# Performance work log

Hardware: AMD Instinct MI355X
Metric: run time of the kernel (lower is better)

## Reference

```python
import jax, jax.numpy as jnp
import numpy as np

DIM = 256
HEADS = 8
HD = DIM // HEADS  # 32
RPE_H = 512
STRIDE = 16
B, NQ = 4, 300
HH, WW = 64, 64
N = HH * WW


def setup_inputs() -> dict:
    key = jax.random.key(0)
    ks = jax.random.split(key, 24)

    def lin(k, fan_in, fan_out):
        return (jax.random.normal(k, (fan_in, fan_out), jnp.float32)
                / np.float32(np.sqrt(fan_in)))

    # boxes in absolute pixel coords (image is WW*STRIDE = 1024 px wide)
    rp_xy = jax.random.uniform(ks[0], (B, NQ, 1, 2), jnp.float32) * (WW * STRIDE)
    rp_wh = jax.random.uniform(ks[1], (B, NQ, 1, 2), jnp.float32) * 256.0 + 16.0
    reference_points = jnp.concatenate([rp_xy, rp_wh], axis=-1)  # [B,NQ,1,4]

    inp = {
        "query": jax.random.normal(ks[2], (B, NQ, DIM), jnp.float32),
        "reference_points": reference_points,
        "k_input_flatten": jax.random.normal(ks[3], (B, N, DIM), jnp.float32),
        "v_input_flatten": jax.random.normal(ks[4], (B, N, DIM), jnp.float32),
        "input_spatial_shapes": jnp.array([[HH, WW]], dtype=jnp.int32),
        "input_padding_mask": (jax.random.uniform(ks[5], (B, N)) < 0.1).astype(jnp.int32),
        # projections (stored as [in, out]; y = x @ W + b)
        "Wq": lin(ks[6], DIM, DIM), "bq": jnp.zeros((DIM,), jnp.float32),
        "Wk": lin(ks[7], DIM, DIM), "bk": jnp.zeros((DIM,), jnp.float32),
        "Wv": lin(ks[8], DIM, DIM), "bv": jnp.zeros((DIM,), jnp.float32),
        "Wp": lin(ks[9], DIM, DIM), "bp": jnp.zeros((DIM,), jnp.float32),
        # CPB MLP 1 (x-deltas): Linear(2,512)+ReLU+Linear(512,HEADS,no bias)
        "W1x": lin(ks[10], 2, RPE_H), "b1x": jnp.zeros((RPE_H,), jnp.float32),
        "W2x": lin(ks[11], RPE_H, HEADS),
        # CPB MLP 2 (y-deltas)
        "W1y": lin(ks[12], 2, RPE_H), "b1y": jnp.zeros((RPE_H,), jnp.float32),
        "W2y": lin(ks[13], RPE_H, HEADS),
    }
    return inp


def reference(query, reference_points, k_input_flatten, v_input_flatten,
              input_spatial_shapes, input_padding_mask,
              Wq, bq, Wk, bk, Wv, bv, Wp, bp,
              W1x, b1x, W2x, W1y, b1y, W2y):
    h = int(input_spatial_shapes[0, 0])
    w = int(input_spatial_shapes[0, 1])
    scale = HD ** -0.5

    # cxcywh -> (x1,y1,x2,y2)
    c, s = reference_points[..., :2], reference_points[..., 2:]
    ref_pts = jnp.concatenate([c - s / 2, c + s / 2], axis=-1)  # [B,NQ,1,4]

    pos_x = (jnp.arange(w, dtype=jnp.float32) + 0.5) * STRIDE  # [w]
    pos_y = (jnp.arange(h, dtype=jnp.float32) + 0.5) * STRIDE  # [h]
    delta_x = ref_pts[..., 0::2] - pos_x[None, None, :, None]  # [B,NQ,w,2]
    delta_y = ref_pts[..., 1::2] - pos_y[None, None, :, None]  # [B,NQ,h,2]

    rpe_x = jax.nn.relu(delta_x @ W1x + b1x) @ W2x  # [B,NQ,w,HEADS]
    rpe_y = jax.nn.relu(delta_y @ W1y + b1y) @ W2y  # [B,NQ,h,HEADS]
    rpe = rpe_x[:, :, None, :, :] + rpe_y[:, :, :, None, :]  # [B,NQ,h,w,H]

    Bq, Nq, C = query.shape
    rpe = rpe.reshape(Bq, Nq, h * w, HEADS).transpose(0, 3, 1, 2)  # [B,H,NQ,N]

    q = (query @ Wq + bq).reshape(Bq, Nq, HEADS, HD).transpose(0, 2, 1, 3) * scale
    k = (k_input_flatten @ Wk + bk).reshape(Bq, -1, HEADS, HD).transpose(0, 2, 1, 3)
    v = (v_input_flatten @ Wv + bv).reshape(Bq, -1, HEADS, HD).transpose(0, 2, 1, 3)

    attn = jnp.einsum('bhqd,bhkd->bhqk', q, k) + rpe
    attn = attn + input_padding_mask[:, None, None, :].astype(attn.dtype) * (-100.0)
    fi = jnp.finfo(attn.dtype)
    attn = jnp.clip(attn, fi.min, fi.max)
    attn = jax.nn.softmax(attn, axis=-1)

    x = jnp.einsum('bhqk,bhkd->bhqd', attn, v)
    x = x.transpose(0, 2, 1, 3).reshape(Bq, Nq, C)
    return x @ Wp + bp
```

## Files before the change

### kernel.cpp

```cpp
#include <hip/hip_runtime.h>
#include <math.h>

#define B_   4
#define NQ_  300
#define DIM_ 256
#define H_   8
#define HD_  32
#define N_   4096

typedef _Float16 f16;
typedef f16   f16x8 __attribute__((ext_vector_type(8)));
typedef f16   f16x4 __attribute__((ext_vector_type(4)));
typedef float f32x4 __attribute__((ext_vector_type(4)));

__global__ __launch_bounds__(256) void prep_wt(
    const float* __restrict__ Wq, const float* __restrict__ Wk,
    const float* __restrict__ Wv, const float* __restrict__ Wp,
    f16* __restrict__ WT, float qscale)
{
  __shared__ float t[64][65];
  const int z = blockIdx.z;
  const float* W = z == 0 ? Wq : z == 1 ? Wk : z == 2 ? Wv : Wp;
  const float s = z == 0 ? qscale : 1.0f;
  f16* O = WT + (size_t)z * 65536;
  const int k0 = blockIdx.y * 64, n0 = blockIdx.x * 64;
  const int r = threadIdx.x >> 2, c0 = (threadIdx.x & 3) * 16;
#pragma unroll
  for (int c = 0; c < 16; c += 4) {
    float4 v = *(const float4*)(W + (size_t)(k0 + r) * 256 + n0 + c0 + c);
    t[r][c0 + c] = v.x; t[r][c0 + c + 1] = v.y;
    t[r][c0 + c + 2] = v.z; t[r][c0 + c + 3] = v.w;
  }
  __syncthreads();
  f16* orow = O + (size_t)(n0 + r) * 256 + k0 + c0;
#pragma unroll
  for (int c = 0; c < 16; c += 4) {
    f16x4 p;
    p[0] = (f16)(t[c0 + c + 0][r] * s);
    p[1] = (f16)(t[c0 + c + 1][r] * s);
    p[2] = (f16)(t[c0 + c + 2][r] * s);
    p[3] = (f16)(t[c0 + c + 3][r] * s);
    *(f16x4*)(orow + c) = p;
  }
}

__device__ __forceinline__ void gemm_body(
    const void* __restrict__ Ain, const f16* __restrict__ WT,
    const float* __restrict__ bias, void* __restrict__ C,
    int M, float scale, int a_f16, int mode, int bm, int bn, int tid)
{
  __shared__ f16 As[64][40];
  __shared__ f16 Bs[64][40];
  const int lane = tid & 63;
  const int wv = tid >> 6;
  const int l15 = lane & 15, g = lane >> 4;
  const int arow = tid >> 2, akq = (tid & 3) * 8;

  f32x4 acc[4];
#pragma unroll
  for (int nt = 0; nt < 4; ++nt) acc[nt] = (f32x4){0.f, 0.f, 0.f, 0.f};

  for (int k0 = 0; k0 < 256; k0 += 32) {
    {
      const int gm = bm + arow;
      f16x8 av;
      if (gm < M) {
        if (a_f16) {
          av = *(const f16x8*)((const f16*)Ain + (size_t)gm * 256 + k0 + akq);
        } else {
          const float* ap = (const float*)Ain + (size_t)gm * 256 + k0 + akq;
          float4 a0 = *(const float4*)ap;
          float4 a1 = *(const float4*)(ap + 4);
          av[0] = (f16)a0.x; av[1] = (f16)a0.y; av[2] = (f16)a0.z; av[3] = (f16)a0.w;
          av[4] = (f16)a1.x; av[5] = (f16)a1.y; av[6] = (f16)a1.z; av[7] = (f16)a1.w;
        }
      } else {
#pragma unroll
        for (int i = 0; i < 8; ++i) av[i] = (f16)0.f;
      }
      *(f16x8*)&As[arow][akq] = av;
      *(f16x8*)&Bs[arow][akq] =
          *(const f16x8*)(WT + (size_t)(bn + arow) * 256 + k0 + akq);
    }
    __syncthreads();
    const f16x8 af = *(const f16x8*)&As[wv * 16 + l15][g * 8];
#pragma unroll
    for (int nt = 0; nt < 4; ++nt) {
      const f16x8 bf = *(const f16x8*)&Bs[nt * 16 + l15][g * 8];
      acc[nt] = __builtin_amdgcn_mfma_f32_16x16x32_f16(af, bf, acc[nt], 0, 0, 0);
    }
    __syncthreads();
  }

#pragma unroll
  for (int nt = 0; nt < 4; ++nt) {
    const int n = bn + nt * 16 + l15;
    const float bv = bias[n] * scale;
    if (mode == 2) {
      const int m0 = bm + wv * 16 + g * 4;
      const int bb = m0 >> 12, nk = m0 & 4095;
      f16x4 pk;
#pragma unroll
      for (int r = 0; r < 4; ++r) pk[r] = (f16)(acc[nt][r] + bv);
      *(f16x4*)((f16*)C + (size_t)bb * (256 * 4096) + (size_t)n * 4096 + nk) = pk;
    } else {
#pragma unroll
      for (int r = 0; r < 4; ++r) {
        const int m = bm + wv * 16 + g * 4 + r;
        if (m >= M) continue;
        const float v = acc[nt][r] + bv;
        if (mode == 0) ((float*)C)[(size_t)m * 256 + n] = v;
        else           ((f16*)C)[(size_t)m * 256 + n] = (f16)v;
      }
    }
  }
}

__global__ __launch_bounds__(256) void proj_qkv(
    const float* __restrict__ query, const float* __restrict__ kin,
    const float* __restrict__ vin, const f16* __restrict__ WT,
    const float* __restrict__ bq, const float* __restrict__ bk,
    const float* __restrict__ bv, f16* __restrict__ Qf,
    f16* __restrict__ Kf, f16* __restrict__ Vtf, float qscale)
{
  const int z = blockIdx.z;
  const int bm = blockIdx.y * 64, bn = blockIdx.x * 64;
  if (z == 0) {
    if (bm >= B_ * NQ_) return;
    gemm_body(query, WT, bq, Qf, B_ * NQ_, qscale, 0, 1, bm, bn, threadIdx.x);
  } else if (z == 1) {
    gemm_body(kin, WT + 65536, bk, Kf, B_ * N_, 1.0f, 0, 1, bm, bn, threadIdx.x);
  } else {
    gemm_body(vin, WT + 2 * 65536, bv, Vtf, B_ * N_, 1.0f, 0, 2, bm, bn, threadIdx.x);
  }
}

__global__ __launch_bounds__(256) void gemm_out(
    const f16* __restrict__ X, const f16* __restrict__ WT,
    const float* __restrict__ bp, float* __restrict__ out)
{
  gemm_body(X, WT + 3 * 65536, bp, out, B_ * NQ_, 1.0f, 1, 0,
            blockIdx.y * 64, blockIdx.x * 64, threadIdx.x);
}

__global__ __launch_bounds__(256) void rpe_kernel(
    const float* __restrict__ refpts,
    const float* __restrict__ W1x, const float* __restrict__ b1x, const float* __restrict__ W2x,
    const float* __restrict__ W1y, const float* __restrict__ b1y, const float* __restrict__ W2y,
    float* __restrict__ rpx, float* __restrict__ rpy)
{
  __shared__ float sRed[4][64][8];
  const int tid = threadIdx.x;
  const int lane = tid & 63;
  const int wv = __builtin_amdgcn_readfirstlane(tid >> 6);
  const int bq = blockIdx.x;
  const int axis = blockIdx.y;
  const float* W1 = axis ? W1y : W1x;
  const float* b1 = axis ? b1y : b1x;
  const float* W2 = axis ? W2y : W2x;
  float* out = axis ? rpy : rpx;

  const float c  = refpts[bq * 4 + axis];
  const float sz = refpts[bq * 4 + 2 + axis];
  const float pos = (lane + 0.5f) * 16.0f;
  const float d0 = c - 0.5f * sz - pos;
  const float d1 = c + 0.5f * sz - pos;
  float acc[8] = {};
  const int r0 = wv * 128;
#pragma unroll 4
  for (int i = 0; i < 128; ++i) {
    const int r = r0 + i;
    const float w10 = W1[r], w11 = W1[512 + r], bb = b1[r];
    const float hv = fmaxf(fmaf(d0, w10, fmaf(d1, w11, bb)), 0.0f);
    const float* w2r = W2 + r * 8;
#pragma unroll
    for (int hh = 0; hh < 8; ++hh) acc[hh] += hv * w2r[hh];
  }
#pragma unroll
  for (int hh = 0; hh < 8; ++hh) sRed[wv][lane][hh] = acc[hh];
  __syncthreads();
  for (int idx = tid; idx < 512; idx += 256) {
    const int jj = idx >> 3, hh = idx & 7;
    out[(size_t)bq * 512 + idx] =
        sRed[0][jj][hh] + sRed[1][jj][hh] + sRed[2][jj][hh] + sRed[3][jj][hh];
  }
}

__global__ __launch_bounds__(512) void attn_mfma(
    const f16* __restrict__ Qf, const f16* __restrict__ Kf,
    const f16* __restrict__ Vtf, const float* __restrict__ rpx,
    const float* __restrict__ rpy, const int* __restrict__ mask,
    f16* __restrict__ X)
{
  __shared__ float smask[N_];
  __shared__ float srx[16][68];
  __shared__ float sry[16][68];
  __shared__ float mO[7][8][64];
  __shared__ float mlm[7][16];
  __shared__ float mll[7][16];

  const int tid = threadIdx.x;
  const int lane = tid & 63;
  const int kh = tid >> 6;
  const int qb = blockIdx.x % 20;
  const int h  = (blockIdx.x / 20) % H_;
  const int b  = blockIdx.x / (20 * H_);
  const int q0 = qb * 16;
  const float L2E = 1.44269504f;

  {
    const int4* mm4 = (const int4*)(mask + b * N_);
    for (int i = tid; i < N_ / 4; i += 512) {
      int4 mm = mm4[i];
      smask[4 * i + 0] = -100.f * L2E * (float)mm.x;
      smask[4 * i + 1] = -100.f * L2E * (float)mm.y;
      smask[4 * i + 2] = -100.f * L2E * (float)mm.z;
      smask[4 * i + 3] = -100.f * L2E * (float)mm.w;
    }
  }
  for (int i = tid; i < 1024; i += 512) {
    int qq = i >> 6, j = i & 63;
    int qg = q0 + qq; if (qg > NQ_ - 1) qg = NQ_ - 1;
    size_t base = (size_t)(b * NQ_ + qg) * 512 + (size_t)j * 8 + h;
    srx[qq][j] = rpx[base] * L2E;
    sry[qq][j] = rpy[base] * L2E;
  }
  __syncthreads();

  const int l15 = lane & 15, g = lane >> 4;
  const int qrow = q0 + l15;
  const int qq = qrow > NQ_ - 1 ? NQ_ - 1 : qrow;

  const f16x8 qf = *(const f16x8*)(Qf + (size_t)(b * NQ_ + qq) * 256 + h * 32 + g * 8);

  f32x4 O0 = {0.f, 0.f, 0.f, 0.f}, O1 = {0.f, 0.f, 0.f, 0.f};
  float lacc = 0.f;
  float mrun = -1e30f;
  const f16* kb  = Kf + (size_t)b * N_ * 256 + h * 32 + g * 8;
  const f16* v0p = Vtf + (size_t)(b * 256 + h * 32 + l15) * N_ + g * 4;
  const f16* v1p = v0p + (size_t)16 * N_;

  for (int sp = 0; sp < 4; ++sp) {
    const int kbase = kh * 512 + sp * 128;
    f32x4 s2c[8];
    float lmax = -1e30f;
#pragma unroll
    for (int cc = 0; cc < 8; ++cc) {
      const int k0 = kbase + cc * 16;
      f16x8 kf = *(const f16x8*)(kb + (size_t)(k0 + l15) * 256);
      f32x4 S = __builtin_amdgcn_mfma_f32_16x16x32_f16(
          kf, qf, (f32x4){0.f, 0.f, 0.f, 0.f}, 0, 0, 0);
      const float ry2 = sry[l15][k0 >> 6];
      const float4 rx = *(const float4*)&srx[l15][(k0 & 63) + g * 4];
      const float4 sm = *(const float4*)&smask[k0 + g * 4];
      f32x4 s2;
      s2[0] = fmaf(S[0], L2E, rx.x + sm.x + ry2);
      s2[1] = fmaf(S[1], L2E, rx.y + sm.y + ry2);
      s2[2] = fmaf(S[2], L2E, rx.z + sm.z + ry2);
      s2[3] = fmaf(S[3], L2E, rx.w + sm.w + ry2);
      lmax = fmaxf(lmax, fmaxf(fmaxf(s2[0], s2[1]), fmaxf(s2[2], s2[3])));
      s2c[cc] = s2;
    }
    lmax = fmaxf(lmax, __shfl_xor(lmax, 16));
    lmax = fmaxf(lmax, __shfl_xor(lmax, 32));
    const float mnew = fmaxf(mrun, lmax);
    const float f = exp2f(mrun - mnew);
    mrun = mnew;
    lacc *= f;
#pragma unroll
    for (int r = 0; r < 4; ++r) { O0[r] *= f; O1[r] *= f; }
#pragma unroll
    for (int cc = 0; cc < 8; ++cc) {
      const int k0 = kbase + cc * 16;
      f16x4 pf;
      float ls = 0.f;
#pragma unroll
      for (int r = 0; r < 4; ++r) {
        const float pv = exp2f(s2c[cc][r] - mrun);
        ls += pv;
        pf[r] = (f16)pv;
      }
      lacc += ls;
      const f16x4 vf0 = *(const f16x4*)(v0p + k0);
      const f16x4 vf1 = *(const f16x4*)(v1p + k0);
      O0 = __builtin_amdgcn_mfma_f32_16x16x16f16(vf0, pf, O0, 0, 0, 0);
      O1 = __builtin_amdgcn_mfma_f32_16x16x16f16(vf1, pf, O1, 0, 0, 0);
    }
  }

  lacc += __shfl_xor(lacc, 16);
  lacc += __shfl_xor(lacc, 32);

  if (kh > 0) {
#pragma unroll
    for (int r = 0; r < 4; ++r) {
      mO[kh - 1][r][lane] = O0[r];
      mO[kh - 1][4 + r][lane] = O1[r];
    }
    if (lane < 16) {
      mlm[kh - 1][lane] = mrun;
      mll[kh - 1][lane] = lacc;
    }
  }
  __syncthreads();
  if (kh == 0) {
    float ms = mrun;
#pragma unroll
    for (int w = 0; w < 7; ++w) ms = fmaxf(ms, mlm[w][l15]);
    const float f0 = exp2f(mrun - ms);
    float lt = lacc * f0;
    float fw[7];
#pragma unroll
    for (int w = 0; w < 7; ++w) {
      fw[w] = exp2f(mlm[w][l15] - ms);
      lt += mll[w][l15] * fw[w];
    }
    const float rl = 1.0f / lt;
    if (qrow < NQ_) {
      f16* xr = X + (size_t)(b * NQ_ + qrow) * 256 + h * 32;
      f16x4 p0, p1;
#pragma unroll
      for (int r = 0; r < 4; ++r) {
        float o0 = O0[r] * f0, o1 = O1[r] * f0;
#pragma unroll
        for (int w = 0; w < 7; ++w) {
          o0 += mO[w][r][lane] * fw[w];
          o1 += mO[w][4 + r][lane] * fw[w];
        }
        p0[r] = (f16)(o0 * rl);
        p1[r] = (f16)(o1 * rl);
      }
      *(f16x4*)(xr + g * 4) = p0;
      *(f16x4*)(xr + 16 + g * 4) = p1;
    }
  }
}

extern "C" void kernel_launch(void* const* d_in, const int* in_sizes, int n_in,
                              void* d_out, int out_size, void* d_ws, size_t ws_size,
                              hipStream_t stream)
{
  const float* query  = (const float*)d_in[0];
  const float* refpts = (const float*)d_in[1];
  const float* kin    = (const float*)d_in[2];
  const float* vin    = (const float*)d_in[3];
  const int*   mask   = (const int*)d_in[5];
  const float* Wq = (const float*)d_in[6];
  const float* bq = (const float*)d_in[7];
  const float* Wk = (const float*)d_in[8];
  const float* bk = (const float*)d_in[9];
  const float* Wv = (const float*)d_in[10];
  const float* bv = (const float*)d_in[11];
  const float* Wp = (const float*)d_in[12];
  const float* bp = (const float*)d_in[13];
  const float* W1x = (const float*)d_in[14];
  const float* b1x = (const float*)d_in[15];
  const float* W2x = (const float*)d_in[16];
  const float* W1y = (const float*)d_in[17];
  const float* b1y = (const float*)d_in[18];
  const float* W2y = (const float*)d_in[19];

  char* wsb = (char*)d_ws;
  f16*   Qf  = (f16*)(wsb);
  f16*   Kf  = (f16*)(wsb + 622592);
  f16*   Vtf = (f16*)(wsb + 9011200);
  float* rpx = (float*)(wsb + 17399808);
  float* rpy = (float*)(wsb + 19857408);
  f16*   X   = (f16*)(wsb + 22315008);
  f16*   WT  = (f16*)(wsb + 22937600);

  const float scale = 0.17677669529663687f;

  hipLaunchKernelGGL(prep_wt, dim3(4, 4, 4), dim3(256), 0, stream,
                     Wq, Wk, Wv, Wp, WT, scale);
  hipLaunchKernelGGL(rpe_kernel, dim3(B_ * NQ_, 2), dim3(256), 0, stream,
                     refpts, W1x, b1x, W2x, W1y, b1y, W2y, rpx, rpy);
  hipLaunchKernelGGL(proj_qkv, dim3(4, 256, 3), dim3(256), 0, stream,
                     query, kin, vin, WT, bq, bk, bv, Qf, Kf, Vtf, scale);
  hipLaunchKernelGGL(attn_mfma, dim3(B_ * H_ * 20), dim3(512), 0, stream,
                     Qf, Kf, Vtf, rpx, rpy, mask, X);
  hipLaunchKernelGGL(gemm_out, dim3(4, 19), dim3(256), 0, stream,
                     X, WT, bp, (float*)d_out);
}
```

Before: 242.3 us.

## Restructure attention kernel: precomputed mask, transposed RPE, smaller chunks, staged V store

The mask-to-float conversion moves out of the attention kernel into extra prep_wt blocks, so the 16KB per-block shared mask and its per-block rebuild go away. RPE outputs are written head-major and pre-scaled by log2(e), which lets attention load them with float4 reads. The attention loop now processes 64-key chunks and prefetches K, V and the mask into registers ahead of the MFMAs, stores partial outputs as f16 to cut LDS use, and drops to 19 query tiles per head. It also sets a 4-blocks-per-CU launch bound and stages the V-transpose store through LDS for coalesced 16-byte writes. Keeping partial sums in f16 slightly lowers precision, and the register-prefetch pattern may raise register pressure.

New measurement: 241.5 us. No clear change (-0.4%).

```diff
diff --git a/kernel.cpp b/kernel.cpp
--- a/kernel.cpp
+++ b/kernel.cpp
@@ -7,19 +7,35 @@
 #define H_   8
 #define HD_  32
 #define N_   4096
+#define QT_  19
 
 typedef _Float16 f16;
 typedef f16   f16x8 __attribute__((ext_vector_type(8)));
 typedef f16   f16x4 __attribute__((ext_vector_type(4)));
 typedef float f32x4 __attribute__((ext_vector_type(4)));
 
+#define L2E 1.44269504f
+
 __global__ __launch_bounds__(256) void prep_wt(
     const float* __restrict__ Wq, const float* __restrict__ Wk,
     const float* __restrict__ Wv, const float* __restrict__ Wp,
-    f16* __restrict__ WT, float qscale)
-{
+    const int* __restrict__ mask, f16* __restrict__ WT,
+    float* __restrict__ maskf, float qscale)
+{
+  const int z = blockIdx.z;
+  if (z == 4) {
+    const int flat = blockIdx.y * 4 + blockIdx.x;
+    const int idx = flat * 1024 + threadIdx.x * 4;
+    int4 mm = *(const int4*)(mask + idx);
+    float4 o;
+    o.x = -100.f * L2E * (float)mm.x;
+    o.y = -100.f * L2E * (float)mm.y;
+    o.z = -100.f * L2E * (float)mm.z;
+    o.w = -100.f * L2E * (float)mm.w;
+    *(float4*)(maskf + idx) = o;
+    return;
+  }
   __shared__ float t[64][65];
-  const int z = blockIdx.z;
   const float* W = z == 0 ? Wq : z == 1 ? Wk : z == 2 ? Wv : Wp;
   const float s = z == 0 ? qscale : 1.0f;
   f16* O = WT + (size_t)z * 65536;
@@ -51,6 +67,7 @@
 {
   __shared__ f16 As[64][40];
   __shared__ f16 Bs[64][40];
+  __shared__ f16 Ts[64][72];
   const int lane = tid & 63;
   const int wv = tid >> 6;
   const int l15 = lane & 15, g = lane >> 4;
@@ -92,18 +109,26 @@
     __syncthreads();
   }
 
-#pragma unroll
-  for (int nt = 0; nt < 4; ++nt) {
-    const int n = bn + nt * 16 + l15;
-    const float bv = bias[n] * scale;
-    if (mode == 2) {
-      const int m0 = bm + wv * 16 + g * 4;
-      const int bb = m0 >> 12, nk = m0 & 4095;
-      f16x4 pk;
-#pragma unroll
-      for (int r = 0; r < 4; ++r) pk[r] = (f16)(acc[nt][r] + bv);
-      *(f16x4*)((f16*)C + (size_t)bb * (256 * 4096) + (size_t)n * 4096 + nk) = pk;
-    } else {
+  if (mode == 2) {
+#pragma unroll
+    for (int nt = 0; nt < 4; ++nt) {
+      const float bv = bias[bn + nt * 16 + l15];
+#pragma unroll
+      for (int r = 0; r < 4; ++r)
+        Ts[nt * 16 + l15][wv * 16 + g * 4 + r] = (f16)(acc[nt][r] + bv);
+    }
+    __syncthreads();
+    const int nl = tid >> 2, mc = (tid & 3) * 16;
+    const int bb = bm >> 12, nk0 = bm & 4095;
+    f16* dst = (f16*)C + (size_t)bb * (256 * 4096) +
+               (size_t)(bn + nl) * 4096 + nk0 + mc;
+    *(f16x8*)dst = *(const f16x8*)&Ts[nl][mc];
+    *(f16x8*)(dst + 8) = *(const f16x8*)&Ts[nl][mc + 8];
+  } else {
+#pragma unroll
+    for (int nt = 0; nt < 4; ++nt) {
+      const int n = bn + nt * 16 + l15;
+      const float bv = bias[n] * scale;
 #pragma unroll
       for (int r = 0; r < 4; ++r) {
         const int m = bm + wv * 16 + g * 4 + r;
@@ -147,9 +172,9 @@
     const float* __restrict__ refpts,
     const float* __restrict__ W1x, const float* __restrict__ b1x, const float* __restrict__ W2x,
     const float* __restrict__ W1y, const float* __restrict__ b1y, const float* __restrict__ W2y,
-    float* __restrict__ rpx, float* __restrict__ rpy)
-{
-  __shared__ float sRed[4][64][8];
+    float* __restrict__ rpxT, float* __restrict__ rpyT)
+{
+  __shared__ float sRed[4][64][9];
   const int tid = threadIdx.x;
   const int lane = tid & 63;
   const int wv = __builtin_amdgcn_readfirstlane(tid >> 6);
@@ -158,7 +183,8 @@
   const float* W1 = axis ? W1y : W1x;
   const float* b1 = axis ? b1y : b1x;
   const float* W2 = axis ? W2y : W2x;
-  float* out = axis ? rpy : rpx;
+  float* out = axis ? rpyT : rpxT;
+  const int b = bq / NQ_, q = bq % NQ_;
 
   const float c  = refpts[bq * 4 + axis];
   const float sz = refpts[bq * 4 + 2 + axis];
@@ -180,127 +206,111 @@
   for (int hh = 0; hh < 8; ++hh) sRed[wv][lane][hh] = acc[hh];
   __syncthreads();
   for (int idx = tid; idx < 512; idx += 256) {
-    const int jj = idx >> 3, hh = idx & 7;
-    out[(size_t)bq * 512 + idx] =
-        sRed[0][jj][hh] + sRed[1][jj][hh] + sRed[2][jj][hh] + sRed[3][jj][hh];
-  }
-}
-
-__global__ __launch_bounds__(512) void attn_mfma(
+    const int hh = idx >> 6, jj = idx & 63;
+    out[((size_t)(b * H_ + hh) * NQ_ + q) * 64 + jj] =
+        (sRed[0][jj][hh] + sRed[1][jj][hh] + sRed[2][jj][hh] + sRed[3][jj][hh]) * L2E;
+  }
+}
+
+__global__ __launch_bounds__(512, 4) void attn_mfma(
     const f16* __restrict__ Qf, const f16* __restrict__ Kf,
-    const f16* __restrict__ Vtf, const float* __restrict__ rpx,
-    const float* __restrict__ rpy, const int* __restrict__ mask,
+    const f16* __restrict__ Vtf, const float* __restrict__ rpxT,
+    const float* __restrict__ rpyT, const float* __restrict__ maskf,
     f16* __restrict__ X)
 {
-  __shared__ float smask[N_];
   __shared__ float srx[16][68];
   __shared__ float sry[16][68];
-  __shared__ float mO[7][8][64];
+  __shared__ f16x4 mO4[7][2][64];
   __shared__ float mlm[7][16];
   __shared__ float mll[7][16];
 
   const int tid = threadIdx.x;
   const int lane = tid & 63;
   const int kh = tid >> 6;
-  const int qb = blockIdx.x % 20;
-  const int h  = (blockIdx.x / 20) % H_;
-  const int b  = blockIdx.x / (20 * H_);
+  const int qb = blockIdx.x % QT_;
+  const int h  = (blockIdx.x / QT_) % H_;
+  const int b  = blockIdx.x / (QT_ * H_);
   const int q0 = qb * 16;
-  const float L2E = 1.44269504f;
 
   {
-    const int4* mm4 = (const int4*)(mask + b * N_);
-    for (int i = tid; i < N_ / 4; i += 512) {
-      int4 mm = mm4[i];
-      smask[4 * i + 0] = -100.f * L2E * (float)mm.x;
-      smask[4 * i + 1] = -100.f * L2E * (float)mm.y;
-      smask[4 * i + 2] = -100.f * L2E * (float)mm.z;
-      smask[4 * i + 3] = -100.f * L2E * (float)mm.w;
-    }
-  }
-  for (int i = tid; i < 1024; i += 512) {
-    int qq = i >> 6, j = i & 63;
+    const int t = tid & 255;
+    const int qq = t >> 4, j4 = t & 15;
     int qg = q0 + qq; if (qg > NQ_ - 1) qg = NQ_ - 1;
-    size_t base = (size_t)(b * NQ_ + qg) * 512 + (size_t)j * 8 + h;
-    srx[qq][j] = rpx[base] * L2E;
-    sry[qq][j] = rpy[base] * L2E;
+    const float* src = (tid < 256 ? rpxT : rpyT) +
+        ((size_t)((b * H_ + h) * NQ_ + qg)) * 64 + j4 * 4;
+    float4 v = *(const float4*)src;
+    float* dst = (tid < 256) ? &srx[qq][j4 * 4] : &sry[qq][j4 * 4];
+    *(float4*)dst = v;
   }
   __syncthreads();
 
   const int l15 = lane & 15, g = lane >> 4;
   const int qrow = q0 + l15;
-  const int qq = qrow > NQ_ - 1 ? NQ_ - 1 : qrow;
-
-  const f16x8 qf = *(const f16x8*)(Qf + (size_t)(b * NQ_ + qq) * 256 + h * 32 + g * 8);
+  const int qc = qrow > NQ_ - 1 ? NQ_ - 1 : qrow;
+  const f16x8 qf = *(const f16x8*)(Qf + (size_t)(b * NQ_ + qc) * 256 + h * 32 + g * 8);
 
   f32x4 O0 = {0.f, 0.f, 0.f, 0.f}, O1 = {0.f, 0.f, 0.f, 0.f};
-  float lacc = 0.f;
-  float mrun = -1e30f;
+  float lacc = 0.f, mrun = -1e30f;
   const f16* kb  = Kf + (size_t)b * N_ * 256 + h * 32 + g * 8;
   const f16* v0p = Vtf + (size_t)(b * 256 + h * 32 + l15) * N_ + g * 4;
   const f16* v1p = v0p + (size_t)16 * N_;
-
-  for (int sp = 0; sp < 4; ++sp) {
-    const int kbase = kh * 512 + sp * 128;
-    f32x4 s2c[8];
-    float lmax = -1e30f;
-#pragma unroll
-    for (int cc = 0; cc < 8; ++cc) {
-      const int k0 = kbase + cc * 16;
-      f16x8 kf = *(const f16x8*)(kb + (size_t)(k0 + l15) * 256);
+  const float* mb = maskf + b * N_;
+
+  for (int sp = 0; sp < 8; ++sp) {
+    const int kbase = kh * 512 + sp * 64;
+    f16x8 kf[4]; f16x4 va[4], vb[4]; float4 m4[4];
+#pragma unroll
+    for (int cc = 0; cc < 4; ++cc) {
+      kf[cc] = *(const f16x8*)(kb + (size_t)(kbase + cc * 16 + l15) * 256);
+      va[cc] = *(const f16x4*)(v0p + kbase + cc * 16);
+      vb[cc] = *(const f16x4*)(v1p + kbase + cc * 16);
+      m4[cc] = *(const float4*)(mb + kbase + cc * 16 + g * 4);
+    }
+    const float ryc = sry[l15][kbase >> 6];
+    f32x4 s[4];
+    float lm = -1e30f;
+#pragma unroll
+    for (int cc = 0; cc < 4; ++cc) {
       f32x4 S = __builtin_amdgcn_mfma_f32_16x16x32_f16(
-          kf, qf, (f32x4){0.f, 0.f, 0.f, 0.f}, 0, 0, 0);
-      const float ry2 = sry[l15][k0 >> 6];
-      const float4 rx = *(const float4*)&srx[l15][(k0 & 63) + g * 4];
-      const float4 sm = *(const float4*)&smask[k0 + g * 4];
-      f32x4 s2;
-      s2[0] = fmaf(S[0], L2E, rx.x + sm.x + ry2);
-      s2[1] = fmaf(S[1], L2E, rx.y + sm.y + ry2);
-      s2[2] = fmaf(S[2], L2E, rx.z + sm.z + ry2);
-      s2[3] = fmaf(S[3], L2E, rx.w + sm.w + ry2);
-      lmax = fmaxf(lmax, fmaxf(fmaxf(s2[0], s2[1]), fmaxf(s2[2], s2[3])));
-      s2c[cc] = s2;
-    }
-    lmax = fmaxf(lmax, __shfl_xor(lmax, 16));
-    lmax = fmaxf(lmax, __shfl_xor(lmax, 32));
-    const float mnew = fmaxf(mrun, lmax);
-    const float f = exp2f(mrun - mnew);
-    mrun = mnew;
-    lacc *= f;
-#pragma unroll
-    for (int r = 0; r < 4; ++r) { O0[r] *= f; O1[r] *= f; }
-#pragma unroll
-    for (int cc = 0; cc < 8; ++cc) {
-      const int k0 = kbase + cc * 16;
+          kf[cc], qf, (f32x4){0.f, 0.f, 0.f, 0.f}, 0, 0, 0);
+      const float4 rx = *(const float4*)&srx[l15][cc * 16 + g * 4];
+      s[cc][0] = fmaf(S[0], L2E, rx.x + m4[cc].x + ryc);
+      s[cc][1] = fmaf(S[1], L2E, rx.y + m4[cc].y + ryc);
+      s[cc][2] = fmaf(S[2], L2E, rx.z + m4[cc].z + ryc);
+      s[cc][3] = fmaf(S[3], L2E, rx.w + m4[cc].w + ryc);
+      lm = fmaxf(lm, fmaxf(fmaxf(s[cc][0], s[cc][1]), fmaxf(s[cc][2], s[cc][3])));
+    }
+    lm = fmaxf(lm, __shfl_xor(lm, 16));
+    lm = fmaxf(lm, __shfl_xor(lm, 32));
+    const float mn = fmaxf(mrun, lm);
+    const float fr = exp2f(mrun - mn);
+    mrun = mn;
+    lacc *= fr;
+#pragma unroll
+    for (int r = 0; r < 4; ++r) { O0[r] *= fr; O1[r] *= fr; }
+#pragma unroll
+    for (int cc = 0; cc < 4; ++cc) {
       f16x4 pf;
-      float ls = 0.f;
 #pragma unroll
       for (int r = 0; r < 4; ++r) {
-        const float pv = exp2f(s2c[cc][r] - mrun);
-        ls += pv;
-        pf[r] = (f16)pv;
+        const float p = exp2f(s[cc][r] - mrun);
+        lacc += p;
+        pf[r] = (f16)p;
       }
-      lacc += ls;
-      const f16x4 vf0 = *(const f16x4*)(v0p + k0);
-      const f16x4 vf1 = *(const f16x4*)(v1p + k0);
-      O0 = __builtin_amdgcn_mfma_f32_16x16x16f16(vf0, pf, O0, 0, 0, 0);
-      O1 = __builtin_amdgcn_mfma_f32_16x16x16f16(vf1, pf, O1, 0, 0, 0);
-    }
-  }
-
+      O0 = __builtin_amdgcn_mfma_f32_16x16x16f16(va[cc], pf, O0, 0, 0, 0);
+      O1 = __builtin_amdgcn_mfma_f32_16x16x16f16(vb[cc], pf, O1, 0, 0, 0);
+    }
+  }
   lacc += __shfl_xor(lacc, 16);
   lacc += __shfl_xor(lacc, 32);
 
   if (kh > 0) {
-#pragma unroll
-    for (int r = 0; r < 4; ++r) {
-      mO[kh - 1][r][lane] = O0[r];
-      mO[kh - 1][4 + r][lane] = O1[r];
-    }
-    if (lane < 16) {
-      mlm[kh - 1][lane] = mrun;
-      mll[kh - 1][lane] = lacc;
-    }
+    f16x4 pa, pb;
+#pragma unroll
+    for (int r = 0; r < 4; ++r) { pa[r] = (f16)O0[r]; pb[r] = (f16)O1[r]; }
+    mO4[kh - 1][0][lane] = pa;
+    mO4[kh - 1][1][lane] = pb;
+    if (lane < 16) { mlm[kh - 1][lane] = mrun; mll[kh - 1][lane] = lacc; }
   }
   __syncthreads();
   if (kh == 0) {
@@ -324,8 +334,8 @@
         float o0 = O0[r] * f0, o1 = O1[r] * f0;
 #pragma unroll
         for (int w = 0; w < 7; ++w) {
-          o0 += mO[w][r][lane] * fw[w];
-          o1 += mO[w][4 + r][lane] * fw[w];
+          o0 += (float)mO4[w][0][lane][r] * fw[w];
+          o1 += (float)mO4[w][1][lane][r] * fw[w];
         }
         p0[r] = (f16)(o0 * rl);
         p1[r] = (f16)(o1 * rl);
@@ -361,24 +371,25 @@
   const float* W2y = (const float*)d_in[19];
 
   char* wsb = (char*)d_ws;
-  f16*   Qf  = (f16*)(wsb);
-  f16*   Kf  = (f16*)(wsb + 622592);
-  f16*   Vtf = (f16*)(wsb + 9011200);
-  float* rpx = (float*)(wsb + 17399808);
-  float* rpy = (float*)(wsb + 19857408);
-  f16*   X   = (f16*)(wsb + 22315008);
-  f16*   WT  = (f16*)(wsb + 22937600);
+  f16*   Qf    = (f16*)(wsb);
+  f16*   Kf    = (f16*)(wsb + 622592);
+  f16*   Vtf   = (f16*)(wsb + 9011200);
+  float* rpxT  = (float*)(wsb + 17399808);
+  float* rpyT  = (float*)(wsb + 19857408);
+  f16*   X     = (f16*)(wsb + 22315008);
+  f16*   WT    = (f16*)(wsb + 22937600);
+  float* maskf = (float*)(wsb + 23461888);
 
   const float scale = 0.17677669529663687f;
 
-  hipLaunchKernelGGL(prep_wt, dim3(4, 4, 4), dim3(256), 0, stream,
-                     Wq, Wk, Wv, Wp, WT, scale);
+  hipLaunchKernelGGL(prep_wt, dim3(4, 4, 5), dim3(256), 0, stream,
+                     Wq, Wk, Wv, Wp, mask, WT, maskf, scale);
   hipLaunchKernelGGL(rpe_kernel, dim3(B_ * NQ_, 2), dim3(256), 0, stream,
-                     refpts, W1x, b1x, W2x, W1y, b1y, W2y, rpx, rpy);
+                     refpts, W1x, b1x, W2x, W1y, b1y, W2y, rpxT, rpyT);
   hipLaunchKernelGGL(proj_qkv, dim3(4, 256, 3), dim3(256), 0, stream,
                      query, kin, vin, WT, bq, bk, bv, Qf, Kf, Vtf, scale);
-  hipLaunchKernelGGL(attn_mfma, dim3(B_ * H_ * 20), dim3(512), 0, stream,
-                     Qf, Kf, Vtf, rpx, rpy, mask, X);
+  hipLaunchKernelGGL(attn_mfma, dim3(B_ * H_ * QT_), dim3(512), 0, stream,
+                     Qf, Kf, Vtf, rpxT, rpyT, maskf, X);
   hipLaunchKernelGGL(gemm_out, dim3(4, 19), dim3(256), 0, stream,
                      X, WT, bp, (float*)d_out);
 }
```
